# Optimization experiments

Measured on AMD Instinct MI355X. Metric: run time of the kernel, lower is better.

Reference implementation:

```python
import jax, jax.numpy as jnp
import numpy as np

N_NODES = 100000
N_EDGES = 3200000
D_NODE = 32
D_EDGE = 6


def _mlp2(x, W1, b1, W2, b2):
    # Linear -> ReLU -> Linear -> ReLU
    h = jax.nn.relu(x @ W1 + b1)
    return jax.nn.relu(h @ W2 + b2)


def setup_inputs() -> dict:
    key = jax.random.key(0)
    ks = jax.random.split(key, 12)
    glorot = lambda k, fi, fo: jax.random.normal(k, (fi, fo), jnp.float32) * (2.0 / (fi + fo)) ** 0.5
    return {
        "x_node": jax.random.normal(ks[0], (N_NODES, D_NODE), jnp.float32),
        "x_edge": jax.random.normal(ks[1], (N_EDGES, D_EDGE), jnp.float32),
        "src": jax.random.randint(ks[2], (N_EDGES,), 0, N_NODES, jnp.int32),
        "dst": jax.random.randint(ks[3], (N_EDGES,), 0, N_NODES, jnp.int32),
        # edge_msg_encoder: 70 -> 32 -> 6
        "We1": glorot(ks[4], 70, 32), "be1": jnp.zeros((32,), jnp.float32),
        "We2": glorot(ks[5], 32, 6), "be2": jnp.zeros((6,), jnp.float32),
        # node_msg_encoder: 38 -> 64 -> 32
        "Wn1": glorot(ks[6], 38, 64), "bn1": jnp.zeros((64,), jnp.float32),
        "Wn2": glorot(ks[7], 64, 32), "bn2": jnp.zeros((32,), jnp.float32),
    }


def reference(x_node, x_edge, src, dst, We1, be1, We2, be2, Wn1, bn1, Wn2, bn2):
    # Gather endpoint node features per edge
    x_dst = x_node[dst]                                   # [E, 32]
    x_src = x_node[src]                                   # [E, 32]
    edge_in = jnp.concatenate([x_dst, x_src, x_edge], 1)  # [E, 70]
    edge_msg = _mlp2(edge_in, We1, be1, We2, be2)         # [E, 6]
    node_in = jnp.concatenate([x_dst, edge_msg], 1)       # [E, 38]
    node_msg = _mlp2(node_in, Wn1, bn1, Wn2, bn2)         # [E, 32]
    # reduce_udf: sum of incoming messages per destination node
    nm = jax.ops.segment_sum(node_msg, dst, num_segments=N_NODES)  # [N, 32]
    return nm, edge_msg
```

## Files before the change

### kernel.cpp

```cpp
#include <hip/hip_runtime.h>

#define N_EDGES 3200000
#define N_NODES 100000

__device__ inline unsigned short f2bf(float f) {
    unsigned u = __float_as_uint(f);
    u += 0x7fffu + ((u >> 16) & 1u);
    return (unsigned short)(u >> 16);
}
__device__ inline unsigned pack_bf2(float lo, float hi) {
    return (unsigned)f2bf(lo) | ((unsigned)f2bf(hi) << 16);
}
__device__ inline float bflo(unsigned u) { return __uint_as_float(u << 16); }
__device__ inline float bfhi(unsigned u) { return __uint_as_float(u & 0xffff0000u); }

__global__ void __launch_bounds__(256) mpn_precompute(
    const float* __restrict__ x_node,
    const float* __restrict__ We1, const float* __restrict__ be1,
    const float* __restrict__ Wn1, const float* __restrict__ bn1,
    unsigned* __restrict__ Pd, unsigned* __restrict__ Ps)
{
    const int n = blockIdx.x * 256 + threadIdx.x;
    if (n >= N_NODES) return;

    float x[32];
    {
        const float4* px = (const float4*)(x_node + (size_t)n * 32);
        #pragma unroll
        for (int i = 0; i < 8; ++i) {
            float4 v = px[i];
            x[4*i+0] = v.x; x[4*i+1] = v.y; x[4*i+2] = v.z; x[4*i+3] = v.w;
        }
    }

    float p1[32];
    #pragma unroll
    for (int j = 0; j < 32; ++j) p1[j] = be1[j];
    for (int k = 0; k < 32; ++k) {
        const float a = x[k];
        const float* w = We1 + k * 32;
        #pragma unroll
        for (int j = 0; j < 32; ++j) p1[j] = fmaf(a, w[j], p1[j]);
    }
    unsigned* pd = Pd + (size_t)n * 48;
    #pragma unroll
    for (int i = 0; i < 16; ++i) pd[i] = pack_bf2(p1[2*i], p1[2*i+1]);

    float p3[64];
    #pragma unroll
    for (int j = 0; j < 64; ++j) p3[j] = bn1[j];
    for (int k = 0; k < 32; ++k) {
        const float a = x[k];
        const float* w = Wn1 + k * 64;
        #pragma unroll
        for (int j = 0; j < 64; ++j) p3[j] = fmaf(a, w[j], p3[j]);
    }
    #pragma unroll
    for (int i = 0; i < 32; ++i) pd[16 + i] = pack_bf2(p3[2*i], p3[2*i+1]);

    float p2[32];
    #pragma unroll
    for (int j = 0; j < 32; ++j) p2[j] = 0.0f;
    for (int k = 0; k < 32; ++k) {
        const float a = x[k];
        const float* w = We1 + (32 + k) * 32;
        #pragma unroll
        for (int j = 0; j < 32; ++j) p2[j] = fmaf(a, w[j], p2[j]);
    }
    unsigned* ps = Ps + (size_t)n * 16;
    #pragma unroll
    for (int i = 0; i < 16; ++i) ps[i] = pack_bf2(p2[2*i], p2[2*i+1]);
}

__global__ void __launch_bounds__(256) mpn_main(
    const unsigned* __restrict__ Pd,
    const unsigned* __restrict__ Ps,
    const float* __restrict__ x_edge,
    const int* __restrict__ src,
    const int* __restrict__ dst,
    const float* __restrict__ We1,
    const float* __restrict__ We2, const float* __restrict__ be2,
    const float* __restrict__ Wn1,
    const float* __restrict__ Wn2, const float* __restrict__ bn2,
    float* __restrict__ nm_out,
    float* __restrict__ em_out)
{
    __shared__ float s_nm[128][33];
    __shared__ int   s_dst[128];

    const int tid = threadIdx.x;
    const int e = blockIdx.x * 256 + tid;
    const int d = dst[e];
    const int s = src[e];

    const uint4* pdrow = (const uint4*)(Pd + (size_t)d * 48);
    const uint4* psrow = (const uint4*)(Ps + (size_t)s * 16);

    float h1[32];
    #pragma unroll
    for (int i = 0; i < 4; ++i) {
        uint4 va = pdrow[i];
        uint4 vb = psrow[i];
        h1[8*i+0] = bflo(va.x) + bflo(vb.x);
        h1[8*i+1] = bfhi(va.x) + bfhi(vb.x);
        h1[8*i+2] = bflo(va.y) + bflo(vb.y);
        h1[8*i+3] = bfhi(va.y) + bfhi(vb.y);
        h1[8*i+4] = bflo(va.z) + bflo(vb.z);
        h1[8*i+5] = bfhi(va.z) + bfhi(vb.z);
        h1[8*i+6] = bflo(va.w) + bflo(vb.w);
        h1[8*i+7] = bfhi(va.w) + bfhi(vb.w);
    }
    float xe[6];
    {
        const float2* pe = (const float2*)(x_edge + (size_t)e * 6);
        float2 a = pe[0], b = pe[1], c = pe[2];
        xe[0]=a.x; xe[1]=a.y; xe[2]=b.x; xe[3]=b.y; xe[4]=c.x; xe[5]=c.y;
    }
    #pragma unroll
    for (int k = 0; k < 6; ++k) {
        const float a = xe[k];
        const float* w = We1 + (64 + k) * 32;
        #pragma unroll
        for (int j = 0; j < 32; ++j) h1[j] = fmaf(a, w[j], h1[j]);
    }
    #pragma unroll
    for (int j = 0; j < 32; ++j) h1[j] = fmaxf(h1[j], 0.0f);

    float em[6];
    #pragma unroll
    for (int j = 0; j < 6; ++j) em[j] = be2[j];
    for (int k = 0; k < 32; ++k) {
        const float a = h1[k];
        const float* w = We2 + k * 6;
        #pragma unroll
        for (int j = 0; j < 6; ++j) em[j] = fmaf(a, w[j], em[j]);
    }
    #pragma unroll
    for (int j = 0; j < 6; ++j) em[j] = fmaxf(em[j], 0.0f);

    {
        float2* eo = (float2*)(em_out + (size_t)e * 6);
        eo[0] = make_float2(em[0], em[1]);
        eo[1] = make_float2(em[2], em[3]);
        eo[2] = make_float2(em[4], em[5]);
    }

    float h2[64];
    #pragma unroll
    for (int i = 0; i < 8; ++i) {
        uint4 v = pdrow[4 + i];
        h2[8*i+0] = bflo(v.x); h2[8*i+1] = bfhi(v.x);
        h2[8*i+2] = bflo(v.y); h2[8*i+3] = bfhi(v.y);
        h2[8*i+4] = bflo(v.z); h2[8*i+5] = bfhi(v.z);
        h2[8*i+6] = bflo(v.w); h2[8*i+7] = bfhi(v.w);
    }
    #pragma unroll
    for (int k = 0; k < 6; ++k) {
        const float a = em[k];
        const float* w = Wn1 + (32 + k) * 64;
        #pragma unroll
        for (int j = 0; j < 64; ++j) h2[j] = fmaf(a, w[j], h2[j]);
    }
    #pragma unroll
    for (int j = 0; j < 64; ++j) h2[j] = fmaxf(h2[j], 0.0f);

    float nm[32];
    #pragma unroll
    for (int j = 0; j < 32; ++j) nm[j] = bn2[j];
    for (int k = 0; k < 64; ++k) {
        const float a = h2[k];
        const float* w = Wn2 + k * 32;
        #pragma unroll
        for (int j = 0; j < 32; ++j) nm[j] = fmaf(a, w[j], nm[j]);
    }

    #pragma unroll
    for (int chunk = 0; chunk < 2; ++chunk) {
        __syncthreads();
        if ((tid >> 7) == chunk) {
            const int lt = tid & 127;
            s_dst[lt] = d;
            #pragma unroll
            for (int j = 0; j < 32; ++j) s_nm[lt][j] = fmaxf(nm[j], 0.0f);
        }
        __syncthreads();
        #pragma unroll 4
        for (int it = 0; it < 16; ++it) {
            const int f  = it * 256 + tid;
            const int le = f >> 5;
            const int j  = f & 31;
            atomicAdd(nm_out + (size_t)s_dst[le] * 32 + j, s_nm[le][j]);
        }
    }
}

extern "C" void kernel_launch(void* const* d_in, const int* in_sizes, int n_in,
                              void* d_out, int out_size, void* d_ws, size_t ws_size,
                              hipStream_t stream) {
    const float* x_node = (const float*)d_in[0];
    const float* x_edge = (const float*)d_in[1];
    const int*   src    = (const int*)d_in[2];
    const int*   dst    = (const int*)d_in[3];
    const float* We1 = (const float*)d_in[4];
    const float* be1 = (const float*)d_in[5];
    const float* We2 = (const float*)d_in[6];
    const float* be2 = (const float*)d_in[7];
    const float* Wn1 = (const float*)d_in[8];
    const float* bn1 = (const float*)d_in[9];
    const float* Wn2 = (const float*)d_in[10];
    const float* bn2 = (const float*)d_in[11];

    float* nm_out = (float*)d_out;
    float* em_out = (float*)d_out + (size_t)N_NODES * 32;

    unsigned* Pd = (unsigned*)d_ws;
    unsigned* Ps = Pd + (size_t)N_NODES * 48;

    hipMemsetAsync(nm_out, 0, (size_t)N_NODES * 32 * sizeof(float), stream);

    mpn_precompute<<<(N_NODES + 255) / 256, 256, 0, stream>>>(
        x_node, We1, be1, Wn1, bn1, Pd, Ps);

    mpn_main<<<N_EDGES / 256, 256, 0, stream>>>(
        Pd, Ps, x_edge, src, dst,
        We1, We2, be2, Wn1, Wn2, bn2,
        nm_out, em_out);
}
```

Measured before the change: 585.8 us.

## Compute second node-MLP layer with bf16 MFMA and fold output zeroing into precompute

Replaces the per-thread scalar 64x32 FMA loop for the node encoder's second layer with MFMA 16x16x32 bf16 instructions. Each wave stages its ReLU'd hidden activations in shared memory as bf16 and multiplies them against a transposed bf16 copy of Wn2 prepared in the precompute kernel. The output zeroing moves from a separate memset into the precompute kernel. This cuts ALU work and register pressure in the main kernel, but adds bf16 rounding of activations and weights and an extra block-wide sync.

```diff
diff --git a/kernel.cpp b/kernel.cpp
--- a/kernel.cpp
+++ b/kernel.cpp
@@ -2,6 +2,9 @@
 
 #define N_EDGES 3200000
 #define N_NODES 100000
+
+typedef __attribute__((ext_vector_type(8))) short bf16x8;
+typedef __attribute__((ext_vector_type(4))) float f32x4;
 
 __device__ inline unsigned short f2bf(float f) {
     unsigned u = __float_as_uint(f);
@@ -18,10 +21,21 @@
     const float* __restrict__ x_node,
     const float* __restrict__ We1, const float* __restrict__ be1,
     const float* __restrict__ Wn1, const float* __restrict__ bn1,
-    unsigned* __restrict__ Pd, unsigned* __restrict__ Ps)
+    const float* __restrict__ Wn2,
+    unsigned* __restrict__ Pd, unsigned* __restrict__ Ps,
+    short* __restrict__ Wn2T,
+    float* __restrict__ nm_out)
 {
     const int n = blockIdx.x * 256 + threadIdx.x;
     if (n >= N_NODES) return;
+
+    {
+        float4 z = make_float4(0.f, 0.f, 0.f, 0.f);
+        float4* o = (float4*)(nm_out + (size_t)n * 32);
+        #pragma unroll
+        for (int i = 0; i < 8; ++i) o[i] = z;
+    }
+    if (n < 2048) Wn2T[n] = (short)f2bf(Wn2[(n & 63) * 32 + (n >> 6)]);
 
     float x[32];
     {
@@ -81,14 +95,20 @@
     const float* __restrict__ We1,
     const float* __restrict__ We2, const float* __restrict__ be2,
     const float* __restrict__ Wn1,
-    const float* __restrict__ Wn2, const float* __restrict__ bn2,
+    const short* __restrict__ Wn2T,
+    const float* __restrict__ bn2,
     float* __restrict__ nm_out,
     float* __restrict__ em_out)
 {
-    __shared__ float s_nm[128][33];
-    __shared__ int   s_dst[128];
-
-    const int tid = threadIdx.x;
+    __shared__ unsigned s_h2[4][64][36];
+    __shared__ int      s_dst[128];
+
+    const int tid  = threadIdx.x;
+    const int lane = tid & 63;
+    const int wave = tid >> 6;
+    const int quad = lane >> 4;
+    const int l15  = lane & 15;
+
     const int e = blockIdx.x * 256 + tid;
     const int d = dst[e];
     const int s = src[e];
@@ -161,27 +181,66 @@
         #pragma unroll
         for (int j = 0; j < 64; ++j) h2[j] = fmaf(a, w[j], h2[j]);
     }
-    #pragma unroll
-    for (int j = 0; j < 64; ++j) h2[j] = fmaxf(h2[j], 0.0f);
-
-    float nm[32];
-    #pragma unroll
-    for (int j = 0; j < 32; ++j) nm[j] = bn2[j];
-    for (int k = 0; k < 64; ++k) {
-        const float a = h2[k];
-        const float* w = Wn2 + k * 32;
-        #pragma unroll
-        for (int j = 0; j < 32; ++j) nm[j] = fmaf(a, w[j], nm[j]);
-    }
-
+
+    {
+        uint4* row = (uint4*)&s_h2[wave][lane][0];
+        #pragma unroll
+        for (int i = 0; i < 8; ++i) {
+            uint4 v;
+            v.x = pack_bf2(fmaxf(h2[8*i+0],0.f), fmaxf(h2[8*i+1],0.f));
+            v.y = pack_bf2(fmaxf(h2[8*i+2],0.f), fmaxf(h2[8*i+3],0.f));
+            v.z = pack_bf2(fmaxf(h2[8*i+4],0.f), fmaxf(h2[8*i+5],0.f));
+            v.w = pack_bf2(fmaxf(h2[8*i+6],0.f), fmaxf(h2[8*i+7],0.f));
+            row[i] = v;
+        }
+    }
+    __syncthreads();
+
+    bf16x8 bfr[2][2];
+    #pragma unroll
+    for (int n = 0; n < 2; ++n)
+        #pragma unroll
+        for (int kt = 0; kt < 2; ++kt)
+            bfr[n][kt] = *(const bf16x8*)(Wn2T + (n*16 + l15)*64 + kt*32 + quad*8);
+
+    f32x4 acc[4][2];
+    #pragma unroll
+    for (int m = 0; m < 4; ++m) { acc[m][0] = (f32x4)0.f; acc[m][1] = (f32x4)0.f; }
+
+    #pragma unroll
+    for (int m = 0; m < 4; ++m) {
+        #pragma unroll
+        for (int kt = 0; kt < 2; ++kt) {
+            bf16x8 af = *(const bf16x8*)((const char*)&s_h2[wave][m*16 + l15][0]
+                                         + kt*64 + quad*16);
+            acc[m][0] = __builtin_amdgcn_mfma_f32_16x16x32_bf16(af, bfr[0][kt], acc[m][0], 0, 0, 0);
+            acc[m][1] = __builtin_amdgcn_mfma_f32_16x16x32_bf16(af, bfr[1][kt], acc[m][1], 0, 0, 0);
+        }
+    }
+
+    const float b0 = bn2[l15];
+    const float b1 = bn2[16 + l15];
+
+    float* s_nm = (float*)s_h2;
     #pragma unroll
     for (int chunk = 0; chunk < 2; ++chunk) {
         __syncthreads();
         if ((tid >> 7) == chunk) {
-            const int lt = tid & 127;
-            s_dst[lt] = d;
+            s_dst[tid & 127] = d;
+            const int be = (wave & 1) * 64;
             #pragma unroll
-            for (int j = 0; j < 32; ++j) s_nm[lt][j] = fmaxf(nm[j], 0.0f);
+            for (int m = 0; m < 4; ++m) {
+                #pragma unroll
+                for (int n = 0; n < 2; ++n) {
+                    const float bb = n ? b1 : b0;
+                    #pragma unroll
+                    for (int r = 0; r < 4; ++r) {
+                        const int le  = be + m*16 + quad*4 + r;
+                        const int out = n*16 + l15;
+                        s_nm[le*33 + out] = fmaxf(acc[m][n][r] + bb, 0.0f);
+                    }
+                }
+            }
         }
         __syncthreads();
         #pragma unroll 4
@@ -189,7 +248,7 @@
             const int f  = it * 256 + tid;
             const int le = f >> 5;
             const int j  = f & 31;
-            atomicAdd(nm_out + (size_t)s_dst[le] * 32 + j, s_nm[le][j]);
+            atomicAdd(nm_out + (size_t)s_dst[le] * 32 + j, s_nm[le*33 + j]);
         }
     }
 }
@@ -213,16 +272,15 @@
     float* nm_out = (float*)d_out;
     float* em_out = (float*)d_out + (size_t)N_NODES * 32;
 
-    unsigned* Pd = (unsigned*)d_ws;
-    unsigned* Ps = Pd + (size_t)N_NODES * 48;
-
-    hipMemsetAsync(nm_out, 0, (size_t)N_NODES * 32 * sizeof(float), stream);
+    unsigned* Pd   = (unsigned*)d_ws;
+    unsigned* Ps   = Pd + (size_t)N_NODES * 48;
+    short*    Wn2T = (short*)(Ps + (size_t)N_NODES * 16);
 
     mpn_precompute<<<(N_NODES + 255) / 256, 256, 0, stream>>>(
-        x_node, We1, be1, Wn1, bn1, Pd, Ps);
+        x_node, We1, be1, Wn1, bn1, Wn2, Pd, Ps, Wn2T, nm_out);
 
     mpn_main<<<N_EDGES / 256, 256, 0, stream>>>(
         Pd, Ps, x_edge, src, dst,
-        We1, We2, be2, Wn1, Wn2, bn2,
+        We1, We2, be2, Wn1, Wn2T, bn2,
         nm_out, em_out);
 }
```

After: 534.0 us. 1.1x faster.
